# Optimization experiments

Hardware: AMD Instinct MI355X
Metric: run time of the kernel (lower is better)

Reference implementation:

```python
import jax, jax.numpy as jnp
import numpy as np
from jax import lax


def get_grid(h, w):
    # normalized [-1,1] grid, channel 0 = x, channel 1 = y, shape [1,h,w,2]
    gx, gy = jnp.meshgrid(jnp.linspace(-1.0, 1.0, w), jnp.linspace(-1.0, 1.0, h))
    return jnp.stack([gx, gy], axis=-1)[None].astype(jnp.float32)


def gaussian_kernel(k, sigma=1.0):
    c = jnp.arange(k, dtype=jnp.float32) - (k - 1) / 2.0
    g = jnp.exp(-(c ** 2) / (2.0 * sigma ** 2))
    k2 = jnp.outer(g, g)
    return k2 / k2.sum()


def resize_bilinear(x, H, W):
    # x: [B,C,h,w]; torch F.interpolate(mode='bilinear', align_corners=False)
    B, C, h, w = x.shape
    def coords(n_out, n_in):
        c = (jnp.arange(n_out, dtype=jnp.float32) + 0.5) * (n_in / n_out) - 0.5
        c = jnp.clip(c, 0.0, n_in - 1.0)
        lo = jnp.floor(c).astype(jnp.int32)
        hi = jnp.minimum(lo + 1, n_in - 1)
        return lo, hi, c - lo.astype(jnp.float32)
    y0, y1, wy = coords(H, h)
    x0, x1, wx = coords(W, w)
    r = x[:, :, y0, :] * (1.0 - wy)[None, None, :, None] + x[:, :, y1, :] * wy[None, None, :, None]
    return r[:, :, :, x0] * (1.0 - wx) + r[:, :, :, x1] * wx


def _forward(src_grid, kernel, src_grid_base, tgt_grid, niter):
    B = src_grid.shape[0]
    H, W = tgt_grid.shape[1], tgt_grid.shape[2]
    ks = kernel.shape[-1]
    HW = H * W
    # forward displacement, resampled to target resolution, in pixel units
    dsrc = (src_grid - src_grid_base).transpose(0, 3, 1, 2)        # [B,2,Hs,Ws]
    dsrc = resize_bilinear(dsrc, H, W)                              # [B,2,H,W]
    dx = dsrc[:, 0].reshape(B, HW) * (W / 2.0)
    dy = dsrc[:, 1].reshape(B, HW) * (H / 2.0)
    xg = (jnp.arange(HW) % W).astype(jnp.float32)
    yg = (jnp.arange(HW) // W).astype(jnp.float32)
    xi = jnp.round(xg[None] + dx).astype(jnp.int32)
    yi = jnp.round(yg[None] + dy).astype(jnp.int32)
    oob = (xi < 0) | (yi < 0) | (xi > W - 1) | (yi > H - 1)
    field = jnp.where(oob, -1, yi * W + xi) + 1   # index 0 = trash slot
    # sort + dedup: duplicates are redirected to the trash slot
    order = jnp.argsort(field, axis=1)            # stable
    sf = jnp.take_along_axis(field, order, axis=1)
    keep = jnp.concatenate([jnp.ones((B, 1), bool), sf[:, 1:] != sf[:, :-1]], axis=1)
    sf = sf * keep
    inv_order = jnp.argsort(order, axis=1)
    field = jnp.take_along_axis(sf, inv_order, axis=1)
    # scatter inverse displacement (unique indices except trash slot 0)
    z = jnp.zeros((B, 1), dtype=dx.dtype)
    dxp = jnp.concatenate([z, dx], axis=1)
    dyp = jnp.concatenate([z, dy], axis=1)
    fieldp = jnp.concatenate([jnp.zeros((B, 1), field.dtype), field], axis=1)
    bidx = jnp.arange(B)[:, None]
    inv_dx = jnp.zeros_like(dxp).at[bidx, fieldp].set(-dxp)[:, 1:].reshape(B, H, W)
    inv_dy = jnp.zeros_like(dyp).at[bidx, fieldp].set(-dyp)[:, 1:].reshape(B, H, W)
    mask = (jnp.zeros_like(dxp).at[bidx, fieldp].set(1.0)[:, 1:].reshape(B, H, W)) > 0.5
    # pad so hole-fill never reads outside
    p = niter + 1
    inv_dx = jnp.pad(inv_dx, ((0, 0), (p, p), (p, p)))
    inv_dy = jnp.pad(inv_dy, ((0, 0), (p, p), (p, p)))
    mask = jnp.pad(mask, ((0, 0), (p, p), (p, p)))
    pd = ks // 2
    k4 = kernel.reshape(1, 1, ks, ks)
    def conv(x):
        return lax.conv_general_dilated(x[:, None], k4, (1, 1), [(pd, pd), (pd, pd)])[:, 0]
    # hole-fill: dilate mask by 4-neighborhood, fill with gaussian-weighted avg
    for _ in range(niter):
        nb = (jnp.pad(mask, ((0, 0), (1, 0), (0, 0)))[:, :-1]
              | jnp.pad(mask, ((0, 0), (0, 1), (0, 0)))[:, 1:]
              | jnp.pad(mask, ((0, 0), (0, 0), (1, 0)))[:, :, :-1]
              | jnp.pad(mask, ((0, 0), (0, 0), (0, 1)))[:, :, 1:])
        new_mask = (~mask) & nb
        new_dx = conv(inv_dx)
        new_dy = conv(inv_dy)
        new_sum = conv(mask.astype(inv_dx.dtype))
        denom = jnp.where(new_mask, new_sum, 1.0)  # safe: new_sum>0 where new_mask
        inv_dx = jnp.where(new_mask, new_dx / denom, inv_dx)
        inv_dy = jnp.where(new_mask, new_dy / denom, inv_dy)
        mask = mask | new_mask
    # erode: drop pixels with any unmasked 4-neighbor (outside counts as masked)
    for _ in range(niter):
        full = (jnp.pad(mask, ((0, 0), (1, 0), (0, 0)), constant_values=True)[:, :-1]
                & jnp.pad(mask, ((0, 0), (0, 1), (0, 0)), constant_values=True)[:, 1:]
                & jnp.pad(mask, ((0, 0), (0, 0), (1, 0)), constant_values=True)[:, :, :-1]
                & jnp.pad(mask, ((0, 0), (0, 0), (0, 1)), constant_values=True)[:, :, 1:])
        mask = mask & full
    inv_dx = jnp.where(mask, inv_dx, 2.0 * W)
    inv_dy = jnp.where(mask, inv_dy, 2.0 * H)
    inv_dx = inv_dx[:, p:-p, p:-p]
    inv_dy = inv_dy[:, p:-p, p:-p]
    dtgt = jnp.stack([inv_dx * (2.0 / W), inv_dy * (2.0 / H)], axis=3)
    return tgt_grid + dtgt


def setup_inputs() -> dict:
    key = jax.random.key(0)
    B, Hs, Ws, H, W = 8, 256, 256, 512, 512
    base = get_grid(Hs, Ws)
    src_grid = base + 0.05 * jax.random.normal(key, (B, Hs, Ws, 2), jnp.float32)
    return {
        "src_grid": src_grid,
        "kernel": gaussian_kernel(3),
        "src_grid_base": base,
        "tgt_grid": get_grid(H, W),
        "niter": 5,
    }


def reference(src_grid, kernel, src_grid_base, tgt_grid, niter):
    return _forward(src_grid, kernel, src_grid_base, tgt_grid, niter)
```

## Files before the change

kernel.cpp:

```cpp
#include <hip/hip_runtime.h>
#include <hip/hip_fp16.h>

typedef unsigned long long u64;
typedef unsigned int u32;
typedef float float4a __attribute__((ext_vector_type(4), aligned(4)));

#define B_    8
#define HS_   256
#define WS_   256
#define H_    512
#define W_    512
#define HW_   (H_ * W_)
#define TO_Y  16
#define NTILE 32
#define WR    36
#define WCOLS 276
#define WSTR  277
#define NBAND 32
#define NBKT  64
#define INFW  0xFFFFFFFFu
#define CAPB  8192

__device__ __forceinline__ void bilin_disp(const float* __restrict__ src,
                                           const float* __restrict__ base,
                                           int b, int y, int x,
                                           float& dx, float& dy) {
#pragma clang fp contract(off)
    float cy = ((float)y + 0.5f) * 0.5f - 0.5f;
    cy = fminf(fmaxf(cy, 0.0f), 255.0f);
    int   y0 = (int)floorf(cy);
    int   y1 = min(y0 + 1, HS_ - 1);
    float wy = cy - (float)y0;

    float cx = ((float)x + 0.5f) * 0.5f - 0.5f;
    cx = fminf(fmaxf(cx, 0.0f), 255.0f);
    int   x0 = (int)floorf(cx);
    float wx = cx - (float)x0;

    float omy = 1.0f - wy;
    float wA, wB;
    int xs;
    if (x0 >= WS_ - 1) { xs = WS_ - 2; wA = 0.0f; wB = 1.0f; }
    else               { xs = x0;      wA = 1.0f - wx; wB = wx; }

    const float4a* S0 = (const float4a*)(src  + ((b * HS_ + y0) * WS_ + xs) * 2);
    const float4a* S1 = (const float4a*)(src  + ((b * HS_ + y1) * WS_ + xs) * 2);
    const float4a* B0 = (const float4a*)(base + (y0 * WS_ + xs) * 2);
    const float4a* B1 = (const float4a*)(base + (y1 * WS_ + xs) * 2);
    float4a s0 = *S0, s1 = *S1, b0 = *B0, b1 = *B1;

    float a00x = s0.x - b0.x, a00y = s0.y - b0.y;
    float a01x = s0.z - b0.z, a01y = s0.w - b0.w;
    float a10x = s1.x - b1.x, a10y = s1.y - b1.y;
    float a11x = s1.z - b1.z, a11y = s1.w - b1.w;

    float r0x = a00x * omy + a10x * wy;
    float r0y = a00y * omy + a10y * wy;
    float r1x = a01x * omy + a11x * wy;
    float r1y = a01y * omy + a11y * wy;
    dx = (r0x * wA + r1x * wB) * 256.0f;
    dy = (r0y * wA + r1y * wB) * 256.0f;
}

__device__ __forceinline__ u32 pack16(float x, float y) {
    __half hx = __float2half_rn(x), hy = __float2half_rn(y);
    return ((u32)__half_as_ushort(hy) << 16) | (u32)__half_as_ushort(hx);
}
__device__ __forceinline__ float2 unpack16(u32 p) {
    float2 f;
    f.x = __half2float(__ushort_as_half((unsigned short)(p & 0xFFFFu)));
    f.y = __half2float(__ushort_as_half((unsigned short)(p >> 16)));
    return f;
}

__device__ __forceinline__ u64 shfl_left(u64 v) {
    unsigned lo = __shfl_up((unsigned)v, 1);
    unsigned hi = __shfl_up((unsigned)(v >> 32), 1);
    u64 r = ((u64)hi << 32) | lo;
    return (threadIdx.x & 63) ? r : 0ull;
}
__device__ __forceinline__ u64 shfl_right(u64 v) {
    unsigned lo = __shfl_down((unsigned)v, 1);
    unsigned hi = __shfl_down((unsigned)(v >> 32), 1);
    u64 r = ((u64)hi << 32) | lo;
    return ((threadIdx.x & 63) == 63) ? 0ull : r;
}

__launch_bounds__(1024)
__global__ void pre_k(const float* __restrict__ src,
                      const float* __restrict__ base,
                      u32* __restrict__ pay,
                      u32* __restrict__ gcount,
                      u32* __restrict__ bucket) {
    __shared__ u32 cnt[NBKT];
    __shared__ u32 bbase[NBKT];

    int bid = blockIdx.x;
    int b   = bid & 7;
    int t   = bid >> 3;
    int j   = t * 1024 + threadIdx.x;
    int y   = j >> 9;
    int x   = j & (W_ - 1);

    if (threadIdx.x < NBKT) cnt[threadIdx.x] = 0;
    __syncthreads();

    float dx, dy;
    bilin_disp(src, base, b, y, x, dx, dy);
    pay[b * HW_ + j] = pack16(-dx, -dy);

    int xi = (int)rintf((float)x + dx);
    int yi = (int)rintf((float)y + dy);
    bool inb = (xi >= 0 && xi < W_ && yi >= 0 && yi < H_);
    int bk0 = 0, bk1 = -1;
    u32 r0 = 0, r1 = 0, e = 0;
    if (inb) {
        int band = yi >> 4;
        bk0 = band * 2 + (xi >> 8);
        r0 = atomicAdd(&cnt[bk0], 1u);
        if      (xi >= 246 && xi <= 255) bk1 = band * 2 + 1;
        else if (xi >= 256 && xi <= 265) bk1 = band * 2;
        if (bk1 >= 0) r1 = atomicAdd(&cnt[bk1], 1u);
        e = ((u32)(yi & 15) << 27) | ((u32)xi << 18) | (u32)j;
    }
    __syncthreads();
    if (threadIdx.x < NBKT) {
        u32 c = cnt[threadIdx.x];
        bbase[threadIdx.x] = c ? atomicAdd(&gcount[b * NBKT + threadIdx.x], c)
                               : 0u;
    }
    __syncthreads();
    if (inb) {
        u32 s0 = bbase[bk0] + r0;
        if (s0 < CAPB) bucket[(b * NBKT + bk0) * CAPB + s0] = e;
        if (bk1 >= 0) {
            u32 s1 = bbase[bk1] + r1;
            if (s1 < CAPB) bucket[(b * NBKT + bk1) * CAPB + s1] = e;
        }
    }
}

__launch_bounds__(512, 2)
__global__ void fused5_k(const u32* __restrict__ pay,
                         const u32* __restrict__ gcount,
                         const u32* __restrict__ bucket,
                         const float* __restrict__ kern,
                         const float* __restrict__ tgt,
                         float* __restrict__ out) {
    __shared__ u32 plane[WR * WSTR];

    int id   = blockIdx.x;
    int b    = id & 7;
    int rest = id >> 3;
    int tile = rest >> 1;
    int half = rest & 1;
    int X0   = half << 8;
    int Y0   = tile * TO_Y;
    int w0   = Y0 - 10;
    int wc0  = X0 - 10;
    int tid  = threadIdx.x;

    float kw[9];
#pragma unroll
    for (int q = 0; q < 9; q++) kw[q] = kern[q];

    for (int i = tid; i < WR * WSTR; i += 512) plane[i] = INFW;
    __syncthreads();

    {
        int qlo = max(0, w0 >> 4);
        int qhi = min(NBAND - 1, (w0 + WR - 1) >> 4);
        for (int q = qlo; q <= qhi; q++) {
            int bki = b * NBKT + q * 2 + half;
            u32 cntq = min(gcount[bki], (u32)CAPB);
            const u32* bk = bucket + bki * CAPB;
            int ybase = q * 16 - w0;
            for (u32 i = tid; i < cntq; i += 512) {
                u32 e  = bk[i];
                int wr = ybase + (int)((e >> 27) & 15u);
                if ((unsigned)wr < WR) {
                    int xc = (int)((e >> 18) & 511u) - wc0;
                    atomicMin(&plane[wr * WSTR + xc], e & 0x3FFFFu);
                }
            }
        }
    }
    __syncthreads();

    int wv   = tid >> 6;
    int lane = tid & 63;
    int col  = X0 + 32 * wv - 16 + lane;
    int cls  = col - wc0;
    bool inwin = ((unsigned)cls < WCOLS);
    bool colin = inwin && (col >= -6) && (col <= W_ + 5);

    u64 m = 0;
    if (colin) {
#pragma unroll 6
        for (int r = 0; r < WR; r++)
            m |= (u64)(plane[r * WSTR + cls] != INFW) << r;
    }
    __syncthreads();

    {
        const u32* pb = pay + b * HW_;
        for (int idx = tid; idx < WR * WCOLS; idx += 512) {
            int rr = idx / WCOLS;
            int cc = idx - rr * WCOLS;
            int off = rr * WSTR + cc;
            u32 k = plane[off];
            plane[off] = (k != INFW) ? pb[k] : 0u;
        }
    }
    __syncthreads();

    int rlo = max(0, -6 - w0);
    int rhi = min(WR - 1, (W_ + 5) - w0);
    u64 validm = colin ? ((((u64)1 << (rhi - rlo + 1)) - 1) << rlo) : 0ull;

    const u64 VROWS = (((u64)1 << 24) - 1) << 6;
    bool vlane = (lane >= 6 && lane <= 57);

    for (int it = 0; it < 5; it++) {
        u64 mL = shfl_left(m), mR = shfl_right(m);
        u64 cand = ~m & ((m << 1) | (m >> 1) | mL | mR) & validm;
        u64 cv = vlane ? (cand & VROWS) : 0ull;
        while (cv) {
            int r = __builtin_ctzll(cv);
            cv &= cv - 1;
            float s = 0.0f, ax = 0.0f, ay = 0.0f;
#pragma unroll
            for (int dr = -1; dr <= 1; dr++) {
#pragma unroll
                for (int dc = -1; dc <= 1; dc++) {
                    if (dr == 0 && dc == 0) continue;
                    u64 nm = (dc < 0) ? mL : ((dc > 0) ? mR : m);
                    float wq = ((nm >> (r + dr)) & 1)
                                 ? kw[(dr + 1) * 3 + (dc + 1)] : 0.0f;
                    int cc = min(max(cls + dc, 0), WCOLS - 1);
                    float2 nv = unpack16(plane[(r + dr) * WSTR + cc]);
                    s += wq; ax += wq * nv.x; ay += wq * nv.y;
                }
            }
            float rs = __builtin_amdgcn_rcpf(s);
            plane[r * WSTR + cls] = pack16(ax * rs, ay * rs);
        }
        m |= cand;
        __syncthreads();
    }

    for (int it = 0; it < 5; it++) {
        u64 mL = shfl_left(m), mR = shfl_right(m);
        m &= (m << 1) & (m >> 1) & mL & mR;
    }

    if (lane >= 16 && lane < 48) {
#pragma unroll 4
        for (int r = 10; r < 10 + TO_Y; r++) {
            int row = w0 + r;
            bool on = (m >> r) & 1;
            float vx, vy;
            if (on) {
                float2 t = unpack16(plane[r * WSTR + cls]);
                vx = t.x * (1.0f / 256.0f);
                vy = t.y * (1.0f / 256.0f);
            } else {
                vx = 4.0f; vy = 4.0f;
            }
            int ti = (row * W_ + col) * 2;
            float2 tg = *(const float2*)(tgt + ti);
            float2 ov; ov.x = tg.x + vx; ov.y = tg.y + vy;
            ((float2*)out)[(size_t)b * HW_ + row * W_ + col] = ov;
        }
    }
}

extern "C" void kernel_launch(void* const* d_in, const int* in_sizes, int n_in,
                              void* d_out, int out_size, void* d_ws, size_t ws_size,
                              hipStream_t stream) {
    const float* src  = (const float*)d_in[0];
    const float* kern = (const float*)d_in[1];
    const float* base = (const float*)d_in[2];
    const float* tgt  = (const float*)d_in[3];
    float* out = (float*)d_out;

    char* ws = (char*)d_ws;
    u32* gcount = (u32*)ws;
    u32* pay    = (u32*)(ws + 4096);
    u32* bucket = (u32*)(ws + 4096 + (size_t)B_ * HW_ * 4);

    hipMemsetAsync(gcount, 0, B_ * NBKT * sizeof(u32), stream);

    pre_k<<<(B_ * HW_) / 1024, 1024, 0, stream>>>(src, base, pay, gcount, bucket);
    fused5_k<<<512, 512, 0, stream>>>(pay, gcount, bucket, kern, tgt, out);
}
```

Baseline: 135.9 us.

## Fuse bucketing and splat kernels into one persistent kernel with grid barrier

Merges the pre-pass and the splat/inpaint kernel into a single persistent 512-block launch separated by a software grid barrier built on an atomic counter. Tiles shrink from half-width to quarter-width (128 columns), with four x-buckets per band and two tile units processed per block, so each block holds a smaller LDS plane and four blocks can share a CU. This removes one kernel launch and the gap between launches. In exchange it depends on all 512 blocks being co-resident for the spin barrier, adds more halo duplication, and leaves half the waves idle in the per-tile phase.

```diff
diff --git a/kernel.cpp b/kernel.cpp
--- a/kernel.cpp
+++ b/kernel.cpp
@@ -12,14 +12,16 @@
 #define W_    512
 #define HW_   (H_ * W_)
 #define TO_Y  16
-#define NTILE 32
 #define WR    36
-#define WCOLS 276
-#define WSTR  277
+#define WCOLS 148
+#define WSTR  149
 #define NBAND 32
-#define NBKT  64
+#define NQ    4
+#define NBKT  (NBAND * NQ)
+#define CAPB  4096
 #define INFW  0xFFFFFFFFu
-#define CAPB  8192
+#define GRID  512
+#define THR   512
 
 __device__ __forceinline__ void bilin_disp(const float* __restrict__ src,
                                            const float* __restrict__ base,
@@ -86,191 +88,220 @@
     return ((threadIdx.x & 63) == 63) ? 0ull : r;
 }
 
-__launch_bounds__(1024)
-__global__ void pre_k(const float* __restrict__ src,
-                      const float* __restrict__ base,
-                      u32* __restrict__ pay,
-                      u32* __restrict__ gcount,
-                      u32* __restrict__ bucket) {
-    __shared__ u32 cnt[NBKT];
-    __shared__ u32 bbase[NBKT];
-
-    int bid = blockIdx.x;
-    int b   = bid & 7;
-    int t   = bid >> 3;
-    int j   = t * 1024 + threadIdx.x;
-    int y   = j >> 9;
-    int x   = j & (W_ - 1);
-
-    if (threadIdx.x < NBKT) cnt[threadIdx.x] = 0;
+__device__ __forceinline__ void grid_bar(u32* bar) {
+    __builtin_amdgcn_fence(__ATOMIC_RELEASE, "agent");
     __syncthreads();
-
-    float dx, dy;
-    bilin_disp(src, base, b, y, x, dx, dy);
-    pay[b * HW_ + j] = pack16(-dx, -dy);
-
-    int xi = (int)rintf((float)x + dx);
-    int yi = (int)rintf((float)y + dy);
-    bool inb = (xi >= 0 && xi < W_ && yi >= 0 && yi < H_);
-    int bk0 = 0, bk1 = -1;
-    u32 r0 = 0, r1 = 0, e = 0;
-    if (inb) {
-        int band = yi >> 4;
-        bk0 = band * 2 + (xi >> 8);
-        r0 = atomicAdd(&cnt[bk0], 1u);
-        if      (xi >= 246 && xi <= 255) bk1 = band * 2 + 1;
-        else if (xi >= 256 && xi <= 265) bk1 = band * 2;
-        if (bk1 >= 0) r1 = atomicAdd(&cnt[bk1], 1u);
-        e = ((u32)(yi & 15) << 27) | ((u32)xi << 18) | (u32)j;
+    if (threadIdx.x == 0) {
+        __hip_atomic_fetch_add(bar, 1u, __ATOMIC_RELAXED, __HIP_MEMORY_SCOPE_AGENT);
+        while (__hip_atomic_load(bar, __ATOMIC_RELAXED, __HIP_MEMORY_SCOPE_AGENT)
+               < (u32)GRID)
+            __builtin_amdgcn_s_sleep(2);
     }
     __syncthreads();
-    if (threadIdx.x < NBKT) {
-        u32 c = cnt[threadIdx.x];
-        bbase[threadIdx.x] = c ? atomicAdd(&gcount[b * NBKT + threadIdx.x], c)
-                               : 0u;
+    __builtin_amdgcn_fence(__ATOMIC_ACQUIRE, "agent");
+}
+
+__launch_bounds__(THR, 4)
+__global__ void warp_k(const float* __restrict__ src,
+                       const float* __restrict__ base,
+                       const float* __restrict__ kern,
+                       const float* __restrict__ tgt,
+                       float* __restrict__ out,
+                       u32* __restrict__ pay,
+                       u32* __restrict__ gcount,
+                       u32* __restrict__ bucket,
+                       u32* __restrict__ bar) {
+    __shared__ u32 plane[WR * WSTR];
+    u32* cntA  = plane;
+    u32* cntB  = plane + NBKT;
+    u32* bbase = plane + 2 * NBKT;
+
+    int sid = blockIdx.x;
+    int tid = threadIdx.x;
+    int b   = sid & 7;
+
+    {
+        if (tid < NBKT) { cntA[tid] = 0; cntB[tid] = 0; }
+        __syncthreads();
+
+        int v = sid >> 3;
+        u32 rec[8];
+#pragma unroll
+        for (int it = 0; it < 8; ++it) {
+            int j = v * 4096 + it * 512 + tid;
+            int y = j >> 9, x = j & (W_ - 1);
+            float dx, dy;
+            bilin_disp(src, base, b, y, x, dx, dy);
+            pay[b * HW_ + j] = pack16(-dx, -dy);
+            int xi = (int)rintf((float)x + dx);
+            int yi = (int)rintf((float)y + dy);
+            bool inb = (xi >= 0 && xi < W_ && yi >= 0 && yi < H_);
+            rec[it] = inb ? (0x80000000u | ((u32)yi << 9) | (u32)xi) : 0u;
+            if (inb) {
+                int bq = xi >> 7;
+                int bk = (yi >> 4) * NQ + bq;
+                atomicAdd(&cntA[bk], 1u);
+                int xm = xi & 127;
+                if      (xm < 10   && bq > 0) atomicAdd(&cntA[bk - 1], 1u);
+                else if (xm >= 118 && bq < 3) atomicAdd(&cntA[bk + 1], 1u);
+            }
+        }
+        __syncthreads();
+        if (tid < NBKT) {
+            u32 c = cntA[tid];
+            bbase[tid] = c ? atomicAdd(&gcount[b * NBKT + tid], c) : 0u;
+        }
+        __syncthreads();
+#pragma unroll
+        for (int it = 0; it < 8; ++it) {
+            u32 r = rec[it];
+            if (r & 0x80000000u) {
+                int xi = (int)(r & 511u);
+                int yi = (int)((r >> 9) & 511u);
+                int j  = v * 4096 + it * 512 + tid;
+                u32 e  = ((u32)(yi & 15) << 27) | ((u32)xi << 18) | (u32)j;
+                int bq = xi >> 7;
+                int bk = (yi >> 4) * NQ + bq;
+                u32 s = bbase[bk] + atomicAdd(&cntB[bk], 1u);
+                if (s < CAPB) bucket[(size_t)(b * NBKT + bk) * CAPB + s] = e;
+                int xm = xi & 127;
+                int bk1 = -1;
+                if      (xm < 10   && bq > 0) bk1 = bk - 1;
+                else if (xm >= 118 && bq < 3) bk1 = bk + 1;
+                if (bk1 >= 0) {
+                    u32 s1 = bbase[bk1] + atomicAdd(&cntB[bk1], 1u);
+                    if (s1 < CAPB) bucket[(size_t)(b * NBKT + bk1) * CAPB + s1] = e;
+                }
+            }
+        }
     }
-    __syncthreads();
-    if (inb) {
-        u32 s0 = bbase[bk0] + r0;
-        if (s0 < CAPB) bucket[(b * NBKT + bk0) * CAPB + s0] = e;
-        if (bk1 >= 0) {
-            u32 s1 = bbase[bk1] + r1;
-            if (s1 < CAPB) bucket[(b * NBKT + bk1) * CAPB + s1] = e;
-        }
-    }
-}
-
-__launch_bounds__(512, 2)
-__global__ void fused5_k(const u32* __restrict__ pay,
-                         const u32* __restrict__ gcount,
-                         const u32* __restrict__ bucket,
-                         const float* __restrict__ kern,
-                         const float* __restrict__ tgt,
-                         float* __restrict__ out) {
-    __shared__ u32 plane[WR * WSTR];
-
-    int id   = blockIdx.x;
-    int b    = id & 7;
-    int rest = id >> 3;
-    int tile = rest >> 1;
-    int half = rest & 1;
-    int X0   = half << 8;
-    int Y0   = tile * TO_Y;
-    int w0   = Y0 - 10;
-    int wc0  = X0 - 10;
-    int tid  = threadIdx.x;
+
+    grid_bar(bar);
 
     float kw[9];
 #pragma unroll
     for (int q = 0; q < 9; q++) kw[q] = kern[q];
 
-    for (int i = tid; i < WR * WSTR; i += 512) plane[i] = INFW;
-    __syncthreads();
-
-    {
-        int qlo = max(0, w0 >> 4);
-        int qhi = min(NBAND - 1, (w0 + WR - 1) >> 4);
-        for (int q = qlo; q <= qhi; q++) {
-            int bki = b * NBKT + q * 2 + half;
-            u32 cntq = min(gcount[bki], (u32)CAPB);
-            const u32* bk = bucket + bki * CAPB;
-            int ybase = q * 16 - w0;
-            for (u32 i = tid; i < cntq; i += 512) {
-                u32 e  = bk[i];
-                int wr = ybase + (int)((e >> 27) & 15u);
-                if ((unsigned)wr < WR) {
-                    int xc = (int)((e >> 18) & 511u) - wc0;
-                    atomicMin(&plane[wr * WSTR + xc], e & 0x3FFFFu);
+    for (int u = 0; u < 2; ++u) {
+        __syncthreads();
+
+        int unit = (u << 9) | sid;
+        int rest = unit >> 3;
+        int tile = rest >> 2;
+        int qx   = rest & 3;
+        int X0   = qx << 7;
+        int Y0   = tile * TO_Y;
+        int w0   = Y0 - 10;
+        int wc0  = X0 - 10;
+
+        for (int i = tid; i < WR * WSTR; i += THR) plane[i] = INFW;
+        __syncthreads();
+
+        {
+            int qlo = max(0, w0 >> 4);
+            int qhi = min(NBAND - 1, (w0 + WR - 1) >> 4);
+            for (int q = qlo; q <= qhi; q++) {
+                int bki = b * NBKT + q * NQ + qx;
+                u32 cntq = min(gcount[bki], (u32)CAPB);
+                const u32* bk = bucket + (size_t)bki * CAPB;
+                int ybase = q * 16 - w0;
+                for (u32 i = tid; i < cntq; i += THR) {
+                    u32 e  = bk[i];
+                    int wr = ybase + (int)((e >> 27) & 15u);
+                    if ((unsigned)wr < WR) {
+                        int xc = (int)((e >> 18) & 511u) - wc0;
+                        atomicMin(&plane[wr * WSTR + xc], e & 0x3FFFFu);
+                    }
                 }
             }
         }
-    }
-    __syncthreads();
-
-    int wv   = tid >> 6;
-    int lane = tid & 63;
-    int col  = X0 + 32 * wv - 16 + lane;
-    int cls  = col - wc0;
-    bool inwin = ((unsigned)cls < WCOLS);
-    bool colin = inwin && (col >= -6) && (col <= W_ + 5);
-
-    u64 m = 0;
-    if (colin) {
+        __syncthreads();
+
+        int wv   = tid >> 6;
+        int lane = tid & 63;
+        int col  = X0 + 32 * wv - 16 + lane;
+        int cls  = col - wc0;
+        bool colin = (wv < 4) && ((unsigned)cls < WCOLS)
+                     && (col >= -6) && (col <= W_ + 5);
+
+        u64 m = 0;
+        if (colin) {
 #pragma unroll 6
-        for (int r = 0; r < WR; r++)
-            m |= (u64)(plane[r * WSTR + cls] != INFW) << r;
-    }
-    __syncthreads();
-
-    {
-        const u32* pb = pay + b * HW_;
-        for (int idx = tid; idx < WR * WCOLS; idx += 512) {
-            int rr = idx / WCOLS;
-            int cc = idx - rr * WCOLS;
-            int off = rr * WSTR + cc;
-            u32 k = plane[off];
-            plane[off] = (k != INFW) ? pb[k] : 0u;
-        }
-    }
-    __syncthreads();
-
-    int rlo = max(0, -6 - w0);
-    int rhi = min(WR - 1, (W_ + 5) - w0);
-    u64 validm = colin ? ((((u64)1 << (rhi - rlo + 1)) - 1) << rlo) : 0ull;
-
-    const u64 VROWS = (((u64)1 << 24) - 1) << 6;
-    bool vlane = (lane >= 6 && lane <= 57);
-
-    for (int it = 0; it < 5; it++) {
-        u64 mL = shfl_left(m), mR = shfl_right(m);
-        u64 cand = ~m & ((m << 1) | (m >> 1) | mL | mR) & validm;
-        u64 cv = vlane ? (cand & VROWS) : 0ull;
-        while (cv) {
-            int r = __builtin_ctzll(cv);
-            cv &= cv - 1;
-            float s = 0.0f, ax = 0.0f, ay = 0.0f;
-#pragma unroll
-            for (int dr = -1; dr <= 1; dr++) {
-#pragma unroll
-                for (int dc = -1; dc <= 1; dc++) {
-                    if (dr == 0 && dc == 0) continue;
-                    u64 nm = (dc < 0) ? mL : ((dc > 0) ? mR : m);
-                    float wq = ((nm >> (r + dr)) & 1)
-                                 ? kw[(dr + 1) * 3 + (dc + 1)] : 0.0f;
-                    int cc = min(max(cls + dc, 0), WCOLS - 1);
-                    float2 nv = unpack16(plane[(r + dr) * WSTR + cc]);
-                    s += wq; ax += wq * nv.x; ay += wq * nv.y;
+            for (int r = 0; r < WR; r++)
+                m |= (u64)(plane[r * WSTR + cls] != INFW) << r;
+        }
+        __syncthreads();
+
+        {
+            const u32* pb = pay + b * HW_;
+            for (int idx = tid; idx < WR * WCOLS; idx += THR) {
+                int rr = idx / WCOLS;
+                int cc = idx - rr * WCOLS;
+                int off = rr * WSTR + cc;
+                u32 k = plane[off];
+                plane[off] = (k != INFW) ? pb[k] : 0u;
+            }
+        }
+        __syncthreads();
+
+        int rlo = max(0, -6 - w0);
+        int rhi = min(WR - 1, (W_ + 5) - w0);
+        u64 validm = colin ? ((((u64)1 << (rhi - rlo + 1)) - 1) << rlo) : 0ull;
+
+        const u64 VROWS = (((u64)1 << 24) - 1) << 6;
+        bool vlane = (lane >= 6 && lane <= 57);
+
+        for (int it = 0; it < 5; it++) {
+            u64 mL = shfl_left(m), mR = shfl_right(m);
+            u64 cand = ~m & ((m << 1) | (m >> 1) | mL | mR) & validm;
+            u64 cv = vlane ? (cand & VROWS) : 0ull;
+            while (cv) {
+                int r = __builtin_ctzll(cv);
+                cv &= cv - 1;
+                float s = 0.0f, ax = 0.0f, ay = 0.0f;
+#pragma unroll
+                for (int dr = -1; dr <= 1; dr++) {
+#pragma unroll
+                    for (int dc = -1; dc <= 1; dc++) {
+                        if (dr == 0 && dc == 0) continue;
+                        u64 nm = (dc < 0) ? mL : ((dc > 0) ? mR : m);
+                        float wq = ((nm >> (r + dr)) & 1)
+                                     ? kw[(dr + 1) * 3 + (dc + 1)] : 0.0f;
+                        int cc = min(max(cls + dc, 0), WCOLS - 1);
+                        float2 nv = unpack16(plane[(r + dr) * WSTR + cc]);
+                        s += wq; ax += wq * nv.x; ay += wq * nv.y;
+                    }
                 }
-            }
-            float rs = __builtin_amdgcn_rcpf(s);
-            plane[r * WSTR + cls] = pack16(ax * rs, ay * rs);
-        }
-        m |= cand;
-        __syncthreads();
-    }
-
-    for (int it = 0; it < 5; it++) {
-        u64 mL = shfl_left(m), mR = shfl_right(m);
-        m &= (m << 1) & (m >> 1) & mL & mR;
-    }
-
-    if (lane >= 16 && lane < 48) {
+                float rs = __builtin_amdgcn_rcpf(s);
+                plane[r * WSTR + cls] = pack16(ax * rs, ay * rs);
+            }
+            m |= cand;
+            __syncthreads();
+        }
+
+        for (int it = 0; it < 5; it++) {
+            u64 mL = shfl_left(m), mR = shfl_right(m);
+            m &= (m << 1) & (m >> 1) & mL & mR;
+        }
+
+        if (colin && lane >= 16 && lane < 48) {
 #pragma unroll 4
-        for (int r = 10; r < 10 + TO_Y; r++) {
-            int row = w0 + r;
-            bool on = (m >> r) & 1;
-            float vx, vy;
-            if (on) {
-                float2 t = unpack16(plane[r * WSTR + cls]);
-                vx = t.x * (1.0f / 256.0f);
-                vy = t.y * (1.0f / 256.0f);
-            } else {
-                vx = 4.0f; vy = 4.0f;
-            }
-            int ti = (row * W_ + col) * 2;
-            float2 tg = *(const float2*)(tgt + ti);
-            float2 ov; ov.x = tg.x + vx; ov.y = tg.y + vy;
-            ((float2*)out)[(size_t)b * HW_ + row * W_ + col] = ov;
+            for (int r = 10; r < 10 + TO_Y; r++) {
+                int row = w0 + r;
+                bool on = (m >> r) & 1;
+                float vx, vy;
+                if (on) {
+                    float2 t = unpack16(plane[r * WSTR + cls]);
+                    vx = t.x * (1.0f / 256.0f);
+                    vy = t.y * (1.0f / 256.0f);
+                } else {
+                    vx = 4.0f; vy = 4.0f;
+                }
+                int ti = (row * W_ + col) * 2;
+                float2 tg = *(const float2*)(tgt + ti);
+                float2 ov; ov.x = tg.x + vx; ov.y = tg.y + vy;
+                ((float2*)out)[(size_t)b * HW_ + row * W_ + col] = ov;
+            }
         }
     }
 }
@@ -285,12 +316,13 @@
     float* out = (float*)d_out;
 
     char* ws = (char*)d_ws;
-    u32* gcount = (u32*)ws;
-    u32* pay    = (u32*)(ws + 4096);
-    u32* bucket = (u32*)(ws + 4096 + (size_t)B_ * HW_ * 4);
-
-    hipMemsetAsync(gcount, 0, B_ * NBKT * sizeof(u32), stream);
-
-    pre_k<<<(B_ * HW_) / 1024, 1024, 0, stream>>>(src, base, pay, gcount, bucket);
-    fused5_k<<<512, 512, 0, stream>>>(pay, gcount, bucket, kern, tgt, out);
-}
+    u32* bar    = (u32*)ws;
+    u32* gcount = (u32*)(ws + 4096);
+    u32* pay    = (u32*)(ws + 65536);
+    u32* bucket = (u32*)(ws + 65536 + (size_t)B_ * HW_ * 4);
+
+    hipMemsetAsync(ws, 0, 65536, stream);
+
+    warp_k<<<GRID, THR, 0, stream>>>(src, base, kern, tgt, out,
+                                     pay, gcount, bucket, bar);
+}
```

Result: slower. 302.2 us (+122.3%).

## Split occupancy bitmap from value plane and shrink value window in LDS

Applied to the files above, without the earlier changes.

Occupancy of the full 36-row window now lives in a separate bitmask array set with atomicOr. Values are kept only for a smaller 26x266 region that the inpainting and output can actually read, so the payload gather and the LDS footprint both shrink. Building the mask from the bitmap removes one barrier. The risk is wrong results if the inner-region bounds miss a cell the 5-iteration fill touches.

```diff
diff --git a/kernel.cpp b/kernel.cpp
--- a/kernel.cpp
+++ b/kernel.cpp
@@ -12,10 +12,12 @@
 #define W_    512
 #define HW_   (H_ * W_)
 #define TO_Y  16
-#define NTILE 32
 #define WR    36
 #define WCOLS 276
-#define WSTR  277
+#define VR    26
+#define VCOLS 266
+#define VSTR  267
+#define OW    9
 #define NBAND 32
 #define NBKT  64
 #define INFW  0xFFFFFFFFu
@@ -147,7 +149,8 @@
                          const float* __restrict__ kern,
                          const float* __restrict__ tgt,
                          float* __restrict__ out) {
-    __shared__ u32 plane[WR * WSTR];
+    __shared__ u32 plane[VR * VSTR + WR * OW];
+    u32* occ = plane + VR * VSTR;
 
     int id   = blockIdx.x;
     int b    = id & 7;
@@ -164,7 +167,8 @@
 #pragma unroll
     for (int q = 0; q < 9; q++) kw[q] = kern[q];
 
-    for (int i = tid; i < WR * WSTR; i += 512) plane[i] = INFW;
+    for (int i = tid; i < VR * VSTR; i += 512) plane[i] = INFW;
+    for (int i = tid; i < WR * OW; i += 512) occ[i] = 0u;
     __syncthreads();
 
     {
@@ -180,7 +184,11 @@
                 int wr = ybase + (int)((e >> 27) & 15u);
                 if ((unsigned)wr < WR) {
                     int xc = (int)((e >> 18) & 511u) - wc0;
-                    atomicMin(&plane[wr * WSTR + xc], e & 0x3FFFFu);
+                    atomicOr(&occ[wr * OW + (xc >> 5)], 1u << (xc & 31));
+                    unsigned vr = (unsigned)(wr - 5);
+                    unsigned vc = (unsigned)(xc - 5);
+                    if (vr < (unsigned)VR && vc < (unsigned)VCOLS)
+                        atomicMin(&plane[vr * VSTR + vc], e & 0x3FFFFu);
                 }
             }
         }
@@ -191,23 +199,24 @@
     int lane = tid & 63;
     int col  = X0 + 32 * wv - 16 + lane;
     int cls  = col - wc0;
-    bool inwin = ((unsigned)cls < WCOLS);
-    bool colin = inwin && (col >= -6) && (col <= W_ + 5);
+    int clsv = cls - 5;
+    bool colin = ((unsigned)cls < WCOLS)
+                 && (col >= -6) && (col <= W_ + 5);
 
     u64 m = 0;
     if (colin) {
+        int wsh = cls & 31, wix = cls >> 5;
 #pragma unroll 6
         for (int r = 0; r < WR; r++)
-            m |= (u64)(plane[r * WSTR + cls] != INFW) << r;
-    }
-    __syncthreads();
+            m |= (u64)((occ[r * OW + wix] >> wsh) & 1u) << r;
+    }
 
     {
         const u32* pb = pay + b * HW_;
-        for (int idx = tid; idx < WR * WCOLS; idx += 512) {
-            int rr = idx / WCOLS;
-            int cc = idx - rr * WCOLS;
-            int off = rr * WSTR + cc;
+        for (int idx = tid; idx < VR * VCOLS; idx += 512) {
+            int rr = idx / VCOLS;
+            int cc = idx - rr * VCOLS;
+            int off = rr * VSTR + cc;
             u32 k = plane[off];
             plane[off] = (k != INFW) ? pb[k] : 0u;
         }
@@ -219,15 +228,17 @@
     u64 validm = colin ? ((((u64)1 << (rhi - rlo + 1)) - 1) << rlo) : 0ull;
 
     const u64 VROWS = (((u64)1 << 24) - 1) << 6;
-    bool vlane = (lane >= 6 && lane <= 57);
+    bool vupd = (lane >= 6 && lane <= 57)
+                && (col >= X0 - 4) && (col <= X0 + 259);
 
     for (int it = 0; it < 5; it++) {
         u64 mL = shfl_left(m), mR = shfl_right(m);
         u64 cand = ~m & ((m << 1) | (m >> 1) | mL | mR) & validm;
-        u64 cv = vlane ? (cand & VROWS) : 0ull;
+        u64 cv = vupd ? (cand & VROWS) : 0ull;
         while (cv) {
             int r = __builtin_ctzll(cv);
             cv &= cv - 1;
+            int rv = r - 5;
             float s = 0.0f, ax = 0.0f, ay = 0.0f;
 #pragma unroll
             for (int dr = -1; dr <= 1; dr++) {
@@ -237,13 +248,13 @@
                     u64 nm = (dc < 0) ? mL : ((dc > 0) ? mR : m);
                     float wq = ((nm >> (r + dr)) & 1)
                                  ? kw[(dr + 1) * 3 + (dc + 1)] : 0.0f;
-                    int cc = min(max(cls + dc, 0), WCOLS - 1);
-                    float2 nv = unpack16(plane[(r + dr) * WSTR + cc]);
+                    int cc = min(max(clsv + dc, 0), VCOLS - 1);
+                    float2 nv = unpack16(plane[(rv + dr) * VSTR + cc]);
                     s += wq; ax += wq * nv.x; ay += wq * nv.y;
                 }
             }
             float rs = __builtin_amdgcn_rcpf(s);
-            plane[r * WSTR + cls] = pack16(ax * rs, ay * rs);
+            plane[rv * VSTR + clsv] = pack16(ax * rs, ay * rs);
         }
         m |= cand;
         __syncthreads();
@@ -261,7 +272,7 @@
             bool on = (m >> r) & 1;
             float vx, vy;
             if (on) {
-                float2 t = unpack16(plane[r * WSTR + cls]);
+                float2 t = unpack16(plane[(r - 5) * VSTR + clsv]);
                 vx = t.x * (1.0f / 256.0f);
                 vy = t.y * (1.0f / 256.0f);
             } else {
```

New measurement: 139.2 us. 1.02x slower.
